# Optimization experiments

Measured on AMD Instinct MI355X. Metric: run time of the kernel, lower is better.

The kernel has to match this reference:

```python
import jax, jax.numpy as jnp
import numpy as np

OUT_FEATURES = 4096
IN_FEATURES = 4096
GROUP_SIZE = 256
NUM_GROUPS = OUT_FEATURES * IN_FEATURES // GROUP_SIZE  # 65536


def setup_inputs() -> dict:
    key = jax.random.key(0)
    k1, k2, k3 = jax.random.split(key, 3)
    x = jax.random.normal(k1, (4, 2048, IN_FEATURES), dtype=jnp.float32)
    weight_packed = jax.random.randint(k2, (NUM_GROUPS, GROUP_SIZE // 2), 0, 256, dtype=jnp.int32)
    # params[..., 0] = scale, params[..., 1] = zero_point; keep scales small like real quant params
    weight_params = jax.random.uniform(k3, (NUM_GROUPS, 2), dtype=jnp.float32) * jnp.array([0.01, 0.1], dtype=jnp.float32)
    return {"x": x, "weight_packed": weight_packed, "weight_params": weight_params}


def _dequantize_4bit(weight_packed, weight_params):
    # weight_packed: [G, gs/2] bytes, two 4-bit values per byte (low nibble = even index)
    scales = weight_params[:, 0:1]  # [G, 1]
    zeros = weight_params[:, 1:2]   # [G, 1]
    low = (weight_packed & 15).astype(jnp.float32)          # even positions
    high = ((weight_packed >> 4) & 15).astype(jnp.float32)  # odd positions
    q = jnp.stack([low, high], axis=-1).reshape(weight_packed.shape[0], -1)  # [G, gs]
    return q * scales + zeros


def reference(x, weight_packed, weight_params):
    w = _dequantize_4bit(weight_packed, weight_params)  # [G, gs]
    w = w.reshape(-1)[: OUT_FEATURES * IN_FEATURES].reshape(OUT_FEATURES, IN_FEATURES)
    # F.linear(x, W) = x @ W.T
    return jnp.einsum("bsi,oi->bso", x, w)
```

## Files before the change

### kernel.cpp

```cpp
#include <hip/hip_runtime.h>
#include <hip/hip_bf16.h>


#define M_DIM 8192
#define N_DIM 4096
#define K_DIM 4096

typedef __bf16 bf16x8 __attribute__((ext_vector_type(8)));
typedef float f32x4 __attribute__((ext_vector_type(4)));

__device__ __forceinline__ unsigned short f2bf_rne(float f) {
    unsigned int u = __builtin_bit_cast(unsigned int, f);
    u += 0x7FFFu + ((u >> 16) & 1u);
    return (unsigned short)(u >> 16);
}

__global__ void convert_x_kernel(const float* __restrict__ x,
                                 ushort* __restrict__ a, int n4) {
    int i = blockIdx.x * blockDim.x + threadIdx.x;
    if (i >= n4) return;
    float4 v = ((const float4*)x)[i];
    ushort4 o;
    o.x = f2bf_rne(v.x);
    o.y = f2bf_rne(v.y);
    o.z = f2bf_rne(v.z);
    o.w = f2bf_rne(v.w);
    ((ushort4*)a)[i] = o;
}

__global__ void dequant_kernel(const int* __restrict__ packed,
                               const float* __restrict__ params,
                               ushort* __restrict__ w, int n) {
    int j = blockIdx.x * blockDim.x + threadIdx.x;
    if (j >= n) return;
    int g = j >> 7;
    int v = packed[j];
    float scale = params[2 * g];
    float zero  = params[2 * g + 1];
    float lo = (float)(v & 15) * scale + zero;
    float hi = (float)((v >> 4) & 15) * scale + zero;
    unsigned int o = (unsigned int)f2bf_rne(lo) | ((unsigned int)f2bf_rne(hi) << 16);
    ((unsigned int*)w)[j] = o;
}

__global__ __launch_bounds__(256, 2) void gemm_bt(const ushort* __restrict__ A,
                                                  const ushort* __restrict__ B,
                                                  float* __restrict__ C) {
    __shared__ __bf16 lds_a[128 * 32];
    __shared__ __bf16 lds_b[128 * 32];

    const int tid  = threadIdx.x;
    const int w    = tid >> 6;
    const int lane = tid & 63;
    const int quad = lane >> 4;
    const int l16  = lane & 15;

    const int m0 = blockIdx.y * 128;
    const int n0 = blockIdx.x * 128;
    const int wm = (w >> 1) * 64;
    const int wn = (w & 1) * 64;

    f32x4 acc[4][4] = {};

    const int row0 = tid >> 2,        col0 = (tid & 3) * 8;
    const int row1 = (256 + tid) >> 2, col1 = (tid & 3) * 8;

    const ushort* aptr0 = A + (size_t)(m0 + row0) * K_DIM + col0;
    const ushort* aptr1 = A + (size_t)(m0 + row1) * K_DIM + col1;
    const ushort* bptr0 = B + (size_t)(n0 + row0) * K_DIM + col0;
    const ushort* bptr1 = B + (size_t)(n0 + row1) * K_DIM + col1;

    __bf16* lda0 = &lds_a[w * 512];
    __bf16* lda1 = &lds_a[2048 + w * 512];
    __bf16* ldb0 = &lds_b[w * 512];
    __bf16* ldb1 = &lds_b[2048 + w * 512];

    for (int k0 = 0; k0 < K_DIM; k0 += 32) {
        __builtin_amdgcn_global_load_lds(
            (const __attribute__((address_space(1))) void*)(aptr0 + k0),
            (__attribute__((address_space(3))) void*)lda0, 16, 0, 0);
        __builtin_amdgcn_global_load_lds(
            (const __attribute__((address_space(1))) void*)(aptr1 + k0),
            (__attribute__((address_space(3))) void*)lda1, 16, 0, 0);
        __builtin_amdgcn_global_load_lds(
            (const __attribute__((address_space(1))) void*)(bptr0 + k0),
            (__attribute__((address_space(3))) void*)ldb0, 16, 0, 0);
        __builtin_amdgcn_global_load_lds(
            (const __attribute__((address_space(1))) void*)(bptr1 + k0),
            (__attribute__((address_space(3))) void*)ldb1, 16, 0, 0);

        __syncthreads();

        bf16x8 af[4], bfv[4];
#pragma unroll
        for (int i = 0; i < 4; ++i) {
            af[i]  = *(const bf16x8*)&lds_a[(wm + i * 16 + l16) * 32 + quad * 8];
            bfv[i] = *(const bf16x8*)&lds_b[(wn + i * 16 + l16) * 32 + quad * 8];
        }
#pragma unroll
        for (int i = 0; i < 4; ++i)
#pragma unroll
            for (int j = 0; j < 4; ++j)
                acc[i][j] = __builtin_amdgcn_mfma_f32_16x16x32_bf16(
                    af[i], bfv[j], acc[i][j], 0, 0, 0);

        __syncthreads();
    }

    const int crow = m0 + wm + quad * 4;
    const int ccol = n0 + wn + l16;
#pragma unroll
    for (int i = 0; i < 4; ++i)
#pragma unroll
        for (int j = 0; j < 4; ++j)
#pragma unroll
            for (int r = 0; r < 4; ++r)
                C[(size_t)(crow + i * 16 + r) * N_DIM + ccol + j * 16] = acc[i][j][r];
}

__global__ void naive_kernel(const float* __restrict__ x, const int* __restrict__ packed,
                             const float* __restrict__ params, float* __restrict__ out) {
    int idx = blockIdx.x * blockDim.x + threadIdx.x;
    if (idx >= M_DIM * N_DIM) return;
    int m = idx / N_DIM, o = idx % N_DIM;
    const float* xr = x + (size_t)m * K_DIM;
    float sum = 0.f;
    for (int gi = 0; gi < K_DIM / 256; ++gi) {
        int g = o * (K_DIM / 256) + gi;
        float s = params[2 * g], z = params[2 * g + 1];
        const int* p = packed + (size_t)g * 128;
        const float* xx = xr + gi * 256;
        for (int j = 0; j < 128; ++j) {
            int v = p[j];
            sum += xx[2 * j]     * ((float)(v & 15) * s + z);
            sum += xx[2 * j + 1] * ((float)((v >> 4) & 15) * s + z);
        }
    }
    out[idx] = sum;
}

extern "C" void kernel_launch(void* const* d_in, const int* in_sizes, int n_in,
                              void* d_out, int out_size, void* d_ws, size_t ws_size,
                              hipStream_t stream) {
    const float* x      = (const float*)d_in[0];
    const int*   packed = (const int*)d_in[1];
    const float* params = (const float*)d_in[2];
    float* out = (float*)d_out;

    const size_t a_bytes = (size_t)M_DIM * K_DIM * 2;
    const size_t w_bytes = (size_t)N_DIM * K_DIM * 2;

    if (ws_size >= a_bytes + w_bytes) {
        ushort* Abf = (ushort*)d_ws;
        ushort* Wbf = (ushort*)((char*)d_ws + a_bytes);

        int n4 = M_DIM * K_DIM / 4;
        convert_x_kernel<<<(n4 + 255) / 256, 256, 0, stream>>>(x, Abf, n4);

        int np = N_DIM * K_DIM / 2;
        dequant_kernel<<<(np + 255) / 256, 256, 0, stream>>>(packed, params, Wbf, np);

        dim3 grid(N_DIM / 128, M_DIM / 128);
        gemm_bt<<<grid, 256, 0, stream>>>(Abf, Wbf, out);
    } else {
        int n = M_DIM * N_DIM;
        naive_kernel<<<(n + 255) / 256, 256, 0, stream>>>(x, packed, params, out);
    }
}
```

Baseline: 544.3 us.

## Merge prep kernels, vectorize conversion, swizzle LDS layout, raise occupancy bound

Replaces the separate x-conversion and dequant kernels with one prep kernel that has each thread process eight elements through 16-byte loads and stores. In the GEMM, the global-to-LDS column placement and the fragment reads are XOR-swizzled to cut LDS bank conflicts on the bf16x8 reads. The launch-bounds occupancy hint rises from 2 to 4 blocks per CU, which may squeeze the register budget for the 64 accumulator floats per lane.

```diff
diff --git a/kernel.cpp b/kernel.cpp
--- a/kernel.cpp
+++ b/kernel.cpp
@@ -8,6 +8,7 @@
 
 typedef __bf16 bf16x8 __attribute__((ext_vector_type(8)));
 typedef float f32x4 __attribute__((ext_vector_type(4)));
+typedef unsigned short us8 __attribute__((ext_vector_type(8)));
 
 __device__ __forceinline__ unsigned short f2bf_rne(float f) {
     unsigned int u = __builtin_bit_cast(unsigned int, f);
@@ -15,35 +16,41 @@
     return (unsigned short)(u >> 16);
 }
 
-__global__ void convert_x_kernel(const float* __restrict__ x,
-                                 ushort* __restrict__ a, int n4) {
-    int i = blockIdx.x * blockDim.x + threadIdx.x;
-    if (i >= n4) return;
-    float4 v = ((const float4*)x)[i];
-    ushort4 o;
-    o.x = f2bf_rne(v.x);
-    o.y = f2bf_rne(v.y);
-    o.z = f2bf_rne(v.z);
-    o.w = f2bf_rne(v.w);
-    ((ushort4*)a)[i] = o;
+__global__ void prep_kernel(const float* __restrict__ x,
+                            const int* __restrict__ packed,
+                            const float* __restrict__ params,
+                            ushort* __restrict__ a,
+                            ushort* __restrict__ w) {
+    int b = blockIdx.x;
+    if (b < 16384) {
+        int j = b * 256 + threadIdx.x;
+        float4 v0 = ((const float4*)x)[2 * j];
+        float4 v1 = ((const float4*)x)[2 * j + 1];
+        us8 o;
+        o[0] = f2bf_rne(v0.x); o[1] = f2bf_rne(v0.y);
+        o[2] = f2bf_rne(v0.z); o[3] = f2bf_rne(v0.w);
+        o[4] = f2bf_rne(v1.x); o[5] = f2bf_rne(v1.y);
+        o[6] = f2bf_rne(v1.z); o[7] = f2bf_rne(v1.w);
+        ((us8*)a)[j] = o;
+    } else {
+        int j = (b - 16384) * 256 + threadIdx.x;
+        int4 v = ((const int4*)packed)[j];
+        int g = j >> 5;
+        float s = params[2 * g], z = params[2 * g + 1];
+        unsigned int o0, o1, o2, o3;
+        o0 = (unsigned int)f2bf_rne((float)(v.x & 15) * s + z)
+           | ((unsigned int)f2bf_rne((float)((v.x >> 4) & 15) * s + z) << 16);
+        o1 = (unsigned int)f2bf_rne((float)(v.y & 15) * s + z)
+           | ((unsigned int)f2bf_rne((float)((v.y >> 4) & 15) * s + z) << 16);
+        o2 = (unsigned int)f2bf_rne((float)(v.z & 15) * s + z)
+           | ((unsigned int)f2bf_rne((float)((v.z >> 4) & 15) * s + z) << 16);
+        o3 = (unsigned int)f2bf_rne((float)(v.w & 15) * s + z)
+           | ((unsigned int)f2bf_rne((float)((v.w >> 4) & 15) * s + z) << 16);
+        ((uint4*)w)[j] = make_uint4(o0, o1, o2, o3);
+    }
 }
 
-__global__ void dequant_kernel(const int* __restrict__ packed,
-                               const float* __restrict__ params,
-                               ushort* __restrict__ w, int n) {
-    int j = blockIdx.x * blockDim.x + threadIdx.x;
-    if (j >= n) return;
-    int g = j >> 7;
-    int v = packed[j];
-    float scale = params[2 * g];
-    float zero  = params[2 * g + 1];
-    float lo = (float)(v & 15) * scale + zero;
-    float hi = (float)((v >> 4) & 15) * scale + zero;
-    unsigned int o = (unsigned int)f2bf_rne(lo) | ((unsigned int)f2bf_rne(hi) << 16);
-    ((unsigned int*)w)[j] = o;
-}
-
-__global__ __launch_bounds__(256, 2) void gemm_bt(const ushort* __restrict__ A,
+__global__ __launch_bounds__(256, 4) void gemm_bt(const ushort* __restrict__ A,
                                                   const ushort* __restrict__ B,
                                                   float* __restrict__ C) {
     __shared__ __bf16 lds_a[128 * 32];
@@ -62,18 +69,22 @@
 
     f32x4 acc[4][4] = {};
 
-    const int row0 = tid >> 2,        col0 = (tid & 3) * 8;
-    const int row1 = (256 + tid) >> 2, col1 = (tid & 3) * 8;
+    const int row0 = tid >> 2;
+    const int row1 = 64 + row0;
+    const int swz  = (tid >> 3) & 3;
+    const int col  = ((tid & 3) ^ swz) * 8;
 
-    const ushort* aptr0 = A + (size_t)(m0 + row0) * K_DIM + col0;
-    const ushort* aptr1 = A + (size_t)(m0 + row1) * K_DIM + col1;
-    const ushort* bptr0 = B + (size_t)(n0 + row0) * K_DIM + col0;
-    const ushort* bptr1 = B + (size_t)(n0 + row1) * K_DIM + col1;
+    const ushort* aptr0 = A + (size_t)(m0 + row0) * K_DIM + col;
+    const ushort* aptr1 = A + (size_t)(m0 + row1) * K_DIM + col;
+    const ushort* bptr0 = B + (size_t)(n0 + row0) * K_DIM + col;
+    const ushort* bptr1 = B + (size_t)(n0 + row1) * K_DIM + col;
 
     __bf16* lda0 = &lds_a[w * 512];
     __bf16* lda1 = &lds_a[2048 + w * 512];
     __bf16* ldb0 = &lds_b[w * 512];
     __bf16* ldb1 = &lds_b[2048 + w * 512];
+
+    const int rq = (quad ^ ((l16 >> 1) & 3)) * 8;
 
     for (int k0 = 0; k0 < K_DIM; k0 += 32) {
         __builtin_amdgcn_global_load_lds(
@@ -94,8 +105,8 @@
         bf16x8 af[4], bfv[4];
 #pragma unroll
         for (int i = 0; i < 4; ++i) {
-            af[i]  = *(const bf16x8*)&lds_a[(wm + i * 16 + l16) * 32 + quad * 8];
-            bfv[i] = *(const bf16x8*)&lds_b[(wn + i * 16 + l16) * 32 + quad * 8];
+            af[i]  = *(const bf16x8*)&lds_a[(wm + i * 16 + l16) * 32 + rq];
+            bfv[i] = *(const bf16x8*)&lds_b[(wn + i * 16 + l16) * 32 + rq];
         }
 #pragma unroll
         for (int i = 0; i < 4; ++i)
@@ -154,11 +165,7 @@
         ushort* Abf = (ushort*)d_ws;
         ushort* Wbf = (ushort*)((char*)d_ws + a_bytes);
 
-        int n4 = M_DIM * K_DIM / 4;
-        convert_x_kernel<<<(n4 + 255) / 256, 256, 0, stream>>>(x, Abf, n4);
-
-        int np = N_DIM * K_DIM / 2;
-        dequant_kernel<<<(np + 255) / 256, 256, 0, stream>>>(packed, params, Wbf, np);
+        prep_kernel<<<24576, 256, 0, stream>>>(x, packed, params, Abf, Wbf);
 
         dim3 grid(N_DIM / 128, M_DIM / 128);
         gemm_bt<<<grid, 256, 0, stream>>>(Abf, Wbf, out);
```

After: 533.4 us. 1.02x faster.
